# Kernel optimization log

Measured on AMD Instinct MI355X. Metric: run time of the kernel, lower is better.

The kernel has to match this reference:

```python
import jax, jax.numpy as jnp
import numpy as np

EPS = 1e-8

def _ste(x, q):
    # straight-through estimator: forward = q, backward = identity
    return x + jax.lax.stop_gradient(q - x)

def quant_act_uint8(x):
    # per-tensor uint8 activation fake-quant (Brevitas Uint8ActPerTensorFloat style)
    s = jax.lax.stop_gradient(jnp.maximum(jnp.max(x), EPS)) / 255.0
    q = jnp.clip(jnp.round(x / s), 0.0, 255.0) * s
    return _ste(x, q), s

def quant_weight_int8_perchannel(w):
    # per-output-channel symmetric int8 fake-quant; w: [out, in]
    s = jax.lax.stop_gradient(jnp.maximum(jnp.max(jnp.abs(w), axis=1, keepdims=True), EPS)) / 127.0
    q = jnp.clip(jnp.round(w / s), -128.0, 127.0) * s
    return _ste(w, q), s[:, 0]

def quant_bias_int32(b, s_in, s_w):
    # bias quantized at scale s_in * s_w[c] (Brevitas Int32Bias)
    s = jax.lax.stop_gradient(s_in * s_w)
    q = jnp.round(b / s) * s
    return _ste(b, q)

def quant_linear(x, w, b):
    xq, s_in = quant_act_uint8(x)
    wq, s_w = quant_weight_int8_perchannel(w)
    bq = quant_bias_int32(b, s_in, s_w)
    return jnp.einsum('btd,fd->btf', xq, wq) + bq

def setup_inputs() -> dict:
    key = jax.random.key(0)
    k1, k2, k3, k4, k5 = jax.random.split(key, 5)
    B, S, D, F = 4, 2048, 1024, 4096
    return {
        'x': jax.random.normal(k1, (B, S, D), dtype=jnp.float32),
        'w1': jax.random.normal(k2, (F, D), dtype=jnp.float32) * (1.0 / np.sqrt(D)),
        'b1': jax.random.normal(k3, (F,), dtype=jnp.float32) * 0.01,
        'w2': jax.random.normal(k4, (D, F), dtype=jnp.float32) * (1.0 / np.sqrt(F)),
        'b2': jax.random.normal(k5, (D,), dtype=jnp.float32) * 0.01,
    }

def reference(x, w1, b1, w2, b2):
    h = jax.nn.relu(quant_linear(x, w1, b1))
    # dropout is identity in eval mode
    return quant_linear(h, w2, b2)
```

## Files before the change

kernel.cpp:

```cpp
#include <hip/hip_runtime.h>
#include <stdint.h>

#define EPSQ 1e-8f

typedef __attribute__((ext_vector_type(4))) int i32x4;

__device__ __forceinline__ unsigned enc_f(float f) {
    unsigned u = __float_as_uint(f);
    return (u & 0x80000000u) ? ~u : (u | 0x80000000u);
}
__device__ __forceinline__ float dec_f(unsigned u) {
    return (u & 0x80000000u) ? __uint_as_float(u & 0x7fffffffu)
                             : __uint_as_float(~u);
}

__device__ __forceinline__ float wave_max_f(float v) {
    #pragma unroll
    for (int off = 32; off; off >>= 1) v = fmaxf(v, __shfl_xor(v, off));
    return v;
}
__device__ __forceinline__ int wave_sum_i(int v) {
    #pragma unroll
    for (int off = 32; off; off >>= 1) v += __shfl_xor(v, off);
    return v;
}

__global__ __launch_bounds__(256) void k_prep(
    const float4* __restrict__ x, long n4x, float* __restrict__ partials,
    const float* __restrict__ w1, signed char* __restrict__ w1q,
    float* __restrict__ sw1, int* __restrict__ rs1,
    const float* __restrict__ w2, signed char* __restrict__ w2q,
    float* __restrict__ sw2, int* __restrict__ rs2) {
    __shared__ float sm[4];
    __shared__ int   si[4];
    int b = blockIdx.x;
    int wid = threadIdx.x >> 6;
    if (b < 2048) {
        long i = (long)b * 256 + threadIdx.x;
        float m = -3.4e38f;
        for (; i < n4x; i += 2048L * 256) {
            float4 v = x[i];
            m = fmaxf(fmaxf(m, fmaxf(v.x, v.y)), fmaxf(v.z, v.w));
        }
        m = wave_max_f(m);
        if ((threadIdx.x & 63) == 0) sm[wid] = m;
        __syncthreads();
        if (threadIdx.x == 0)
            partials[b] = fmaxf(fmaxf(sm[0], sm[1]), fmaxf(sm[2], sm[3]));
        return;
    }
    const float* w; signed char* q; float* s_out; int* rs_out; int row, L;
    if (b < 2048 + 4096) { row = b - 2048; w = w1; q = w1q; s_out = sw1; rs_out = rs1; L = 1024; }
    else                 { row = b - 6144; w = w2; q = w2q; s_out = sw2; rs_out = rs2; L = 4096; }

    const float4* wr = (const float4*)(w + (long)row * L);
    int n4 = L >> 2;
    float m = 0.0f;
    for (int i = threadIdx.x; i < n4; i += 256) {
        float4 v = wr[i];
        m = fmaxf(m, fmaxf(fmaxf(fabsf(v.x), fabsf(v.y)),
                           fmaxf(fabsf(v.z), fabsf(v.w))));
    }
    m = wave_max_f(m);
    if ((threadIdx.x & 63) == 0) sm[wid] = m;
    __syncthreads();
    m = fmaxf(fmaxf(sm[0], sm[1]), fmaxf(sm[2], sm[3]));
    float s = fmaxf(m, EPSQ) / 127.0f;

    char4* qr = (char4*)(q + (long)row * L);
    int isum = 0;
    for (int i = threadIdx.x; i < n4; i += 256) {
        float4 v = wr[i];
        int a = min(max((int)rintf(v.x / s), -128), 127);
        int bb = min(max((int)rintf(v.y / s), -128), 127);
        int c = min(max((int)rintf(v.z / s), -128), 127);
        int d = min(max((int)rintf(v.w / s), -128), 127);
        isum += a + bb + c + d;
        char4 cc; cc.x = (char)a; cc.y = (char)bb; cc.z = (char)c; cc.w = (char)d;
        qr[i] = cc;
    }
    isum = wave_sum_i(isum);
    if ((threadIdx.x & 63) == 0) si[wid] = isum;
    __syncthreads();
    if (threadIdx.x == 0) {
        s_out[row]  = s;
        rs_out[row] = si[0] + si[1] + si[2] + si[3];
    }
}

__global__ __launch_bounds__(256) void k_reduce_max(const float* __restrict__ partials,
                                                    int n, unsigned* __restrict__ slot) {
    __shared__ float sm[4];
    float m = -3.4e38f;
    for (int i = threadIdx.x; i < n; i += 256) m = fmaxf(m, partials[i]);
    m = wave_max_f(m);
    if ((threadIdx.x & 63) == 0) sm[threadIdx.x >> 6] = m;
    __syncthreads();
    if (threadIdx.x == 0)
        *slot = enc_f(fmaxf(fmaxf(sm[0], sm[1]), fmaxf(sm[2], sm[3])));
}

__global__ __launch_bounds__(256) void k_quant_act(const float4* __restrict__ in,
                                                   char4* __restrict__ out, long n4,
                                                   const unsigned* __restrict__ slot) {
    float s = fmaxf(dec_f(*slot), EPSQ) / 255.0f;
    long i = (long)blockIdx.x * 256 + threadIdx.x;
    for (; i < n4; i += (long)gridDim.x * 256) {
        float4 v = in[i];
        int a = min(max((int)rintf(v.x / s), 0), 255) - 128;
        int b = min(max((int)rintf(v.y / s), 0), 255) - 128;
        int c = min(max((int)rintf(v.z / s), 0), 255) - 128;
        int d = min(max((int)rintf(v.w / s), 0), 255) - 128;
        char4 cc; cc.x = (char)a; cc.y = (char)b; cc.z = (char)c; cc.w = (char)d;
        out[i] = cc;
    }
}

__device__ __forceinline__ void gl_lds16(const signed char* g, signed char* l) {
    __builtin_amdgcn_global_load_lds(
        (const __attribute__((address_space(1))) unsigned int*)g,
        (__attribute__((address_space(3))) unsigned int*)l, 16, 0, 0);
}

template<int MODE, int BM, int NW>
__global__ __launch_bounds__(NW * 64, (MODE == 0 ? 3 : 4)) void k_gemm_i8(
    const signed char* __restrict__ A,
    const signed char* __restrict__ B,
    const float* __restrict__ s_w,
    const int* __restrict__ rowsum,
    const float* __restrict__ bias,
    const unsigned* __restrict__ act_slot,
    float* __restrict__ Cf,
    signed char* __restrict__ Cq,
    unsigned* __restrict__ omax_slot,
    int M, int N, long K) {
    __shared__ __align__(16) signed char Als[BM * 128];
    __shared__ __align__(16) signed char Bls[128 * 128];
    __shared__ float red[NW];

    const int t    = threadIdx.x;
    const int lane = t & 63;
    const int w    = t >> 6;
    const int m0   = blockIdx.y * BM;
    const int n0   = blockIdx.x * 128;
    const int mr   = lane & 15;
    const int qq   = lane >> 4;
    constexpr int PB = 8 / NW;

    const signed char* a0 = A + (long)(m0 + w * 32 + mr) * K + qq * 16;
    const signed char* b0 = B + (long)(n0 + w * PB * 16 + mr) * K + qq * 16;
    signed char* ad = Als + w * 4096 + lane * 16;
    signed char* bd = Bls + w * PB * 2048 + lane * 16;

    const int wrow = (w >> 1) * 64;
    const int wcol = (w & 1) * 64;
    const int a_base = (w >> 1) * 8192 + lane * 16;
    const int b_base = (w & 1) * 8192 + lane * 16;

    i32x4 acc[4][4];
    #pragma unroll
    for (int i = 0; i < 4; i++)
        #pragma unroll
        for (int j = 0; j < 4; j++) acc[i][j] = (i32x4){0, 0, 0, 0};

    for (long k0 = 0; k0 < K; k0 += 128) {
        __syncthreads();
        gl_lds16(a0 + k0,               ad);
        gl_lds16(a0 + k0 + 64,          ad + 1024);
        gl_lds16(a0 + k0 + 16 * K,      ad + 2048);
        gl_lds16(a0 + k0 + 16 * K + 64, ad + 3072);
        #pragma unroll
        for (int p = 0; p < PB; p++) {
            gl_lds16(b0 + k0 + (long)p * 16 * K,      bd + p * 2048);
            gl_lds16(b0 + k0 + (long)p * 16 * K + 64, bd + p * 2048 + 1024);
        }
        __syncthreads();

        #pragma unroll
        for (int kk = 0; kk < 2; kk++) {
            i32x4 af[4], bf[4];
            #pragma unroll
            for (int i = 0; i < 4; i++)
                af[i] = *(const i32x4*)(Als + a_base + i * 2048 + kk * 1024);
            #pragma unroll
            for (int j = 0; j < 4; j++)
                bf[j] = *(const i32x4*)(Bls + b_base + j * 2048 + kk * 1024);
            #pragma unroll
            for (int i = 0; i < 4; i++)
                #pragma unroll
                for (int j = 0; j < 4; j++)
                    acc[i][j] = __builtin_amdgcn_mfma_i32_16x16x64_i8(
                        af[i], bf[j], acc[i][j], 0, 0, 0);
        }
    }

    const float s_act = fmaxf(dec_f(*act_slot), EPSQ) / 255.0f;

    if (MODE == 1) {
        float lmax = 0.0f;
        #pragma unroll
        for (int j = 0; j < 4; j++) {
            int im = -2147483647 - 1;
            #pragma unroll
            for (int i = 0; i < 4; i++)
                #pragma unroll
                for (int r = 0; r < 4; r++) im = max(im, acc[i][j][r]);
            int gn = n0 + wcol + j * 16 + mr;
            float ssc  = s_act * s_w[gn];
            float bint = rintf(bias[gn] / ssc);
            float h = ssc * ((float)(im + 128 * rowsum[gn]) + bint);
            lmax = fmaxf(lmax, h);
        }
        lmax = fmaxf(lmax, 0.0f);
        lmax = wave_max_f(lmax);
        if (lane == 0) red[w] = lmax;
        __syncthreads();
        if (t == 0) {
            float bm = red[0];
            #pragma unroll
            for (int i = 1; i < NW; i++) bm = fmaxf(bm, red[i]);
            atomicMax(omax_slot, enc_f(bm));
        }
        return;
    }

    float s_oq = 1.0f;
    if (MODE == 2) s_oq = fmaxf(dec_f(*omax_slot), EPSQ) / 255.0f;

    #pragma unroll
    for (int j = 0; j < 4; j++) {
        int gn = n0 + wcol + j * 16 + mr;
        float ssc  = s_act * s_w[gn];
        float bint = rintf(bias[gn] / ssc);
        int   icor = 128 * rowsum[gn];
        float fq   = (MODE == 2) ? (ssc / s_oq) : 0.0f;
        #pragma unroll
        for (int i = 0; i < 4; i++) {
            #pragma unroll
            for (int r = 0; r < 4; r++) {
                int gm = m0 + wrow + i * 16 + qq * 4 + r;
                float v = (float)(acc[i][j][r] + icor) + bint;
                if (MODE == 0) {
                    Cf[(long)gm * N + gn] = ssc * v;
                } else {
                    int qv = min(max((int)rintf(fq * v), 0), 255) - 128;
                    Cq[(long)gm * N + gn] = (signed char)qv;
                }
            }
        }
    }
}

extern "C" void kernel_launch(void* const* d_in, const int* in_sizes, int n_in,
                              void* d_out, int out_size, void* d_ws, size_t ws_size,
                              hipStream_t stream) {
    const float* x  = (const float*)d_in[0];
    const float* w1 = (const float*)d_in[1];
    const float* b1 = (const float*)d_in[2];
    const float* w2 = (const float*)d_in[3];
    const float* b2 = (const float*)d_in[4];
    float* out = (float*)d_out;

    const int M = 8192, D = 1024, F = 4096;

    char* ws = (char*)d_ws;
    size_t off = 0;
    unsigned* slots = (unsigned*)ws;               off += 256;
    float* partials = (float*)(ws + off);          off += 2048 * 4;
    signed char* xi  = (signed char*)(ws + off);   off += (size_t)M * D;
    signed char* w1q = (signed char*)(ws + off);   off += (size_t)F * D;
    signed char* w2q = (signed char*)(ws + off);   off += (size_t)D * F;
    float* sw1 = (float*)(ws + off);               off += (size_t)F * 4;
    float* sw2 = (float*)(ws + off);               off += (size_t)D * 4;
    int* rs1   = (int*)(ws + off);                 off += (size_t)F * 4;
    int* rs2   = (int*)(ws + off);                 off += (size_t)D * 4;
    signed char* hq = (signed char*)(ws + off);    off += (size_t)M * F;

    hipMemsetAsync(slots, 0, 8, stream);

    k_prep<<<dim3(2048 + F + D), dim3(256), 0, stream>>>(
        (const float4*)x, (long)M * D / 4, partials,
        w1, w1q, sw1, rs1, w2, w2q, sw2, rs2);
    k_reduce_max<<<dim3(1), dim3(256), 0, stream>>>(partials, 2048, slots + 0);
    k_quant_act<<<dim3(2048), dim3(256), 0, stream>>>((const float4*)x, (char4*)xi,
                                                      (long)M * D / 4, slots + 0);
    k_gemm_i8<1, 256, 8><<<dim3(F / 128, M / 256), dim3(512), 0, stream>>>(
        xi, w1q, sw1, rs1, b1, slots + 0, nullptr, nullptr, slots + 1, M, F, (long)D);
    k_gemm_i8<2, 256, 8><<<dim3(F / 128, M / 256), dim3(512), 0, stream>>>(
        xi, w1q, sw1, rs1, b1, slots + 0, nullptr, hq, slots + 1, M, F, (long)D);
    k_gemm_i8<0, 128, 4><<<dim3(D / 128, M / 128), dim3(256), 0, stream>>>(
        hq, w2q, sw2, rs2, b2, slots + 1, out, nullptr, nullptr, M, D, (long)F);

    (void)in_sizes; (void)n_in; (void)out_size; (void)ws_size;
}
```

Baseline: 298.1 us.

## Double-buffer LDS tiles to overlap global loads with MFMA compute

Splits the shared A/B tiles into two buffers and prefetches the next K-slice with global_load_lds while MFMAs consume the current one. A manual waitcnt plus a single barrier per step replaces the two syncthreads per iteration. LDS use doubles and launch bounds drop to 2 blocks per SM, which lowers occupancy in exchange for hiding load latency.

```diff
diff --git a/kernel.cpp b/kernel.cpp
--- a/kernel.cpp
+++ b/kernel.cpp
@@ -122,8 +122,22 @@
         (__attribute__((address_space(3))) unsigned int*)l, 16, 0, 0);
 }
 
+template<int PB>
+__device__ __forceinline__ void stage(const signed char* a0, const signed char* b0,
+                                      signed char* ad, signed char* bd, long K) {
+    gl_lds16(a0,               ad);
+    gl_lds16(a0 + 64,          ad + 1024);
+    gl_lds16(a0 + 16 * K,      ad + 2048);
+    gl_lds16(a0 + 16 * K + 64, ad + 3072);
+    #pragma unroll
+    for (int p = 0; p < PB; p++) {
+        gl_lds16(b0 + (long)p * 16 * K,      bd + p * 2048);
+        gl_lds16(b0 + (long)p * 16 * K + 64, bd + p * 2048 + 1024);
+    }
+}
+
 template<int MODE, int BM, int NW>
-__global__ __launch_bounds__(NW * 64, (MODE == 0 ? 3 : 4)) void k_gemm_i8(
+__global__ __launch_bounds__(NW * 64, 2) void k_gemm_i8(
     const signed char* __restrict__ A,
     const signed char* __restrict__ B,
     const float* __restrict__ s_w,
@@ -134,8 +148,8 @@
     signed char* __restrict__ Cq,
     unsigned* __restrict__ omax_slot,
     int M, int N, long K) {
-    __shared__ __align__(16) signed char Als[BM * 128];
-    __shared__ __align__(16) signed char Bls[128 * 128];
+    __shared__ __align__(16) signed char Als[2][BM * 128];
+    __shared__ __align__(16) signed char Bls[2][128 * 128];
     __shared__ float red[NW];
 
     const int t    = threadIdx.x;
@@ -149,8 +163,8 @@
 
     const signed char* a0 = A + (long)(m0 + w * 32 + mr) * K + qq * 16;
     const signed char* b0 = B + (long)(n0 + w * PB * 16 + mr) * K + qq * 16;
-    signed char* ad = Als + w * 4096 + lane * 16;
-    signed char* bd = Bls + w * PB * 2048 + lane * 16;
+    const int ad_off = w * 4096 + lane * 16;
+    const int bd_off = w * PB * 2048 + lane * 16;
 
     const int wrow = (w >> 1) * 64;
     const int wcol = (w & 1) * 64;
@@ -163,34 +177,44 @@
         #pragma unroll
         for (int j = 0; j < 4; j++) acc[i][j] = (i32x4){0, 0, 0, 0};
 
-    for (long k0 = 0; k0 < K; k0 += 128) {
-        __syncthreads();
-        gl_lds16(a0 + k0,               ad);
-        gl_lds16(a0 + k0 + 64,          ad + 1024);
-        gl_lds16(a0 + k0 + 16 * K,      ad + 2048);
-        gl_lds16(a0 + k0 + 16 * K + 64, ad + 3072);
-        #pragma unroll
-        for (int p = 0; p < PB; p++) {
-            gl_lds16(b0 + k0 + (long)p * 16 * K,      bd + p * 2048);
-            gl_lds16(b0 + k0 + (long)p * 16 * K + 64, bd + p * 2048 + 1024);
-        }
-        __syncthreads();
-
+    auto compute = [&](const signed char* Ab, const signed char* Bb) {
         #pragma unroll
         for (int kk = 0; kk < 2; kk++) {
             i32x4 af[4], bf[4];
             #pragma unroll
             for (int i = 0; i < 4; i++)
-                af[i] = *(const i32x4*)(Als + a_base + i * 2048 + kk * 1024);
+                af[i] = *(const i32x4*)(Ab + a_base + i * 2048 + kk * 1024);
             #pragma unroll
             for (int j = 0; j < 4; j++)
-                bf[j] = *(const i32x4*)(Bls + b_base + j * 2048 + kk * 1024);
+                bf[j] = *(const i32x4*)(Bb + b_base + j * 2048 + kk * 1024);
             #pragma unroll
             for (int i = 0; i < 4; i++)
                 #pragma unroll
                 for (int j = 0; j < 4; j++)
                     acc[i][j] = __builtin_amdgcn_mfma_i32_16x16x64_i8(
                         af[i], bf[j], acc[i][j], 0, 0, 0);
+        }
+    };
+
+    const int NIT = (int)(K >> 7);
+    stage<PB>(a0, b0, Als[0] + ad_off, Bls[0] + bd_off, K);
+
+    for (int it = 0; it < NIT; it += 2) {
+        __builtin_amdgcn_s_waitcnt(0x0F70);
+        __syncthreads();
+        __builtin_amdgcn_sched_barrier(0);
+        if (it + 1 < NIT)
+            stage<PB>(a0 + (it + 1) * 128, b0 + (it + 1) * 128,
+                      Als[1] + ad_off, Bls[1] + bd_off, K);
+        compute(Als[0], Bls[0]);
+        if (it + 1 < NIT) {
+            __builtin_amdgcn_s_waitcnt(0x0F70);
+            __syncthreads();
+            __builtin_amdgcn_sched_barrier(0);
+            if (it + 2 < NIT)
+                stage<PB>(a0 + (it + 2) * 128, b0 + (it + 2) * 128,
+                          Als[0] + ad_off, Bls[0] + bd_off, K);
+            compute(Als[1], Bls[1]);
         }
     }
 
```

New measurement: 338.7 us. 13.6% more time.
